# Kernel optimization log

Hardware: AMD Instinct MI355X
Metric: run time of the kernel (lower is better)

The kernel has to match this reference:

```python
import jax, jax.numpy as jnp
import numpy as np

B, L, D, H = 2, 2048, 1024, 16
DH = D // H  # 64


def setup_inputs() -> dict:
    key = jax.random.key(0)
    ks = jax.random.split(key, 9)
    s = 1.0 / np.sqrt(D)
    x = jax.random.normal(ks[0], (B, L, D), dtype=jnp.float32)
    # per-head projection weights stacked on leading head axis (torch Linear: y = x W^T + b)
    Wq = jax.random.normal(ks[1], (H, D, DH), dtype=jnp.float32) * s
    bq = jax.random.normal(ks[2], (H, DH), dtype=jnp.float32) * s
    Wk = jax.random.normal(ks[3], (H, D, DH), dtype=jnp.float32) * s
    bk = jax.random.normal(ks[4], (H, DH), dtype=jnp.float32) * s
    Wv = jax.random.normal(ks[5], (H, D, DH), dtype=jnp.float32) * s
    bv = jax.random.normal(ks[6], (H, DH), dtype=jnp.float32) * s
    WO = jax.random.normal(ks[7], (D, D), dtype=jnp.float32) * s  # torch layout [out, in]
    bO = jax.random.normal(ks[8], (D,), dtype=jnp.float32) * s
    return {"x": x, "Wq": Wq, "bq": bq, "Wk": Wk, "bk": bk,
            "Wv": Wv, "bv": bv, "WO": WO, "bO": bO}


def reference(x, Wq, bq, Wk, bk, Wv, bv, WO, bO):
    # Q,K,V: [B,H,L,DH]
    Q = jnp.einsum('bld,hdk->bhlk', x, Wq) + bq[None, :, None, :]
    K = jnp.einsum('bld,hdk->bhlk', x, Wk) + bk[None, :, None, :]
    V = jnp.einsum('bld,hdk->bhlk', x, Wv) + bv[None, :, None, :]
    scale = 1.0 / jnp.sqrt(jnp.asarray(DH, dtype=x.dtype))
    att = jnp.einsum('bhik,bhjk->bhij', Q, K) * scale  # [B,H,Lq,Lk]
    # NOTE: original softmaxes over dim=1 of [B,Lq,Lk] -> the QUERY axis (axis=2 here)
    att = jax.nn.softmax(att, axis=2)
    # dropout is identity in eval/reference mode
    out = jnp.einsum('bhij,bhjk->bhik', att, V)  # [B,H,L,DH]
    out = out.transpose(0, 2, 1, 3).reshape(B, L, D)  # concat heads on feature axis
    return jnp.einsum('bld,ed->ble', out, WO) + bO
```

## Files before the change

kernel.cpp:

```cpp
#include <hip/hip_runtime.h>
#include <math.h>

#define NB 2
#define NL 2048
#define ND 1024
#define NH 16
#define NDH 64
static constexpr float SCALE = 0.125f;

typedef short          bhalf8 __attribute__((ext_vector_type(8)));
typedef unsigned short ush8   __attribute__((ext_vector_type(8)));
typedef unsigned short ush4   __attribute__((ext_vector_type(4)));
typedef float          f32x4  __attribute__((ext_vector_type(4)));

#define MFMA_BF16(a, b, c) __builtin_amdgcn_mfma_f32_16x16x32_bf16(a, b, c, 0, 0, 0)

__device__ __forceinline__ unsigned short f2bf(float f) {
    unsigned u = __float_as_uint(f);
    u += 0x7FFF + ((u >> 16) & 1);
    return (unsigned short)(u >> 16);
}
__device__ __forceinline__ float bf2f(unsigned short s) {
    return __uint_as_float((unsigned)s << 16);
}
__device__ __forceinline__ unsigned pack_bf16(float lo, float hi) {
    unsigned a = __float_as_uint(lo) + 0x8000u;
    unsigned b = __float_as_uint(hi) + 0x8000u;
    return __builtin_amdgcn_perm(b, a, 0x07060302u);
}
__device__ __forceinline__ void gload16(const unsigned short* g, unsigned short* l) {
    __builtin_amdgcn_global_load_lds(
        (const __attribute__((address_space(1))) unsigned int*)(const void*)g,
        (__attribute__((address_space(3))) unsigned int*)(void*)l,
        16, 0, 0);
}

__global__ __launch_bounds__(256) void k_cvt(
    const float* __restrict__ x, const float* __restrict__ WO,
    unsigned short* __restrict__ xb, unsigned short* __restrict__ wob)
{
    size_t u = (size_t)blockIdx.x * 256 + threadIdx.x;
    const float* src; unsigned short* dst; size_t off;
    if (u < 524288) { src = x;  dst = xb;  off = u * 8; }
    else            { src = WO; dst = wob; off = (u - 524288) * 8; }
    float4 a = *(const float4*)(src + off);
    float4 b = *(const float4*)(src + off + 4);
    uint4 o;
    o.x = pack_bf16(a.x, a.y); o.y = pack_bf16(a.z, a.w);
    o.z = pack_bf16(b.x, b.y); o.w = pack_bf16(b.z, b.w);
    *(uint4*)(dst + off) = o;
}

__global__ __launch_bounds__(256) void k_cvt_wt(
    const float* __restrict__ Wq, const float* __restrict__ Wk,
    const float* __restrict__ Wv, unsigned short* __restrict__ Wtb)
{
    __shared__ unsigned short T[64][72];
    const int d0  = blockIdx.x * 64;
    const int qkv = blockIdx.y >> 4;
    const int h   = blockIdx.y & 15;
    const float* W = (qkv == 0 ? Wq : (qkv == 1 ? Wk : Wv)) + (size_t)h * (ND * NDH);
    const int t = threadIdx.x;
#pragma unroll
    for (int p = 0; p < 4; ++p) {
        int u  = t + p * 256;
        int dr = u >> 4;
        int c4 = (u & 15) * 4;
        float4 v = *(const float4*)(W + (size_t)(d0 + dr) * NDH + c4);
        T[c4 + 0][dr] = f2bf(v.x);
        T[c4 + 1][dr] = f2bf(v.y);
        T[c4 + 2][dr] = f2bf(v.z);
        T[c4 + 3][dr] = f2bf(v.w);
    }
    __syncthreads();
    unsigned short* outp = Wtb + (size_t)(qkv * NH + h) * NDH * ND;
#pragma unroll
    for (int p = 0; p < 2; ++p) {
        int u  = t + p * 256;
        int dh = u >> 3;
        int sg = (u & 7) * 8;
        *(ush8*)(outp + (size_t)dh * ND + d0 + sg) = *(ush8*)&T[dh][sg];
    }
}

__global__ __launch_bounds__(256, 2) void k_qkv_mfma(
    const unsigned short* __restrict__ xb, const unsigned short* __restrict__ Wtb,
    const float* __restrict__ bq, const float* __restrict__ bk,
    const float* __restrict__ bv,
    unsigned short* __restrict__ Qb, unsigned short* __restrict__ Kb,
    unsigned short* __restrict__ Vtb)
{
    __shared__ unsigned short LB[2 * 128 * 64];
    unsigned short* As = LB;
    unsigned short* Bs = LB + 128 * 64;

    const int mt = blockIdx.x;
    const int nt = blockIdx.y;
    const int qkv = nt >> 3;
    const int t = threadIdx.x, w = t >> 6, lane = t & 63;
    const int lr = lane & 15, lg = lane >> 4;
    const int wm = (w >> 1) * 64, wn = (w & 1) * 64;
    const int swz = (lr & 7) << 3;
    const int rA = lane >> 3, cg = (lane & 7) * 8;

    f32x4 acc[4][4] = {};

    for (int k0 = 0; k0 < ND; k0 += 64) {
        __syncthreads();
#pragma unroll
        for (int i = 0; i < 4; ++i) {
            int c  = w * 4 + i;
            int r  = c * 8 + rA;
            int gc = cg ^ ((r & 7) << 3);
            gload16(xb  + (size_t)(mt * 128 + r) * ND + k0 + gc, &As[c * 512]);
            gload16(Wtb + (size_t)(nt * 128 + r) * ND + k0 + gc, &Bs[c * 512]);
        }
        __syncthreads();

        bhalf8 av[4][2], bw[4][2];
#pragma unroll
        for (int f = 0; f < 4; ++f)
#pragma unroll
            for (int ks = 0; ks < 2; ++ks) {
                int c = (ks * 32 + lg * 8) ^ swz;
                av[f][ks] = *(const bhalf8*)&As[(wm + f * 16 + lr) * 64 + c];
                bw[f][ks] = *(const bhalf8*)&Bs[(wn + f * 16 + lr) * 64 + c];
            }
#pragma unroll
        for (int mf = 0; mf < 4; ++mf)
#pragma unroll
            for (int nf = 0; nf < 4; ++nf) {
                acc[mf][nf] = MFMA_BF16(av[mf][0], bw[nf][0], acc[mf][nf]);
                acc[mf][nf] = MFMA_BF16(av[mf][1], bw[nf][1], acc[mf][nf]);
            }
    }

    const float* bias = (qkv == 0 ? bq : (qkv == 1 ? bk : bv));
    const int nb = (nt & 7) * 128;
    float bi[4];
#pragma unroll
    for (int nf = 0; nf < 4; ++nf) bi[nf] = bias[nb + wn + nf * 16 + lr];

    __syncthreads();
    unsigned short* TS = LB;

    if (qkv < 2) {
#pragma unroll
        for (int mf = 0; mf < 4; ++mf)
#pragma unroll
            for (int nf = 0; nf < 4; ++nf)
#pragma unroll
                for (int r = 0; r < 4; ++r) {
                    int m = wm + mf * 16 + lg * 4 + r;
                    int n = (wn + nf * 16 + lr) ^ ((m & 7) << 3);
                    TS[m * 128 + n] = f2bf(acc[mf][nf][r] + bi[nf]);
                }
        __syncthreads();
        unsigned short* outp = (qkv == 0 ? Qb : Kb);
#pragma unroll
        for (int p = 0; p < 8; ++p) {
            int u = t + p * 256;
            int r = u >> 4, sg = (u & 15) * 8;
            ush8 v = *(const ush8*)&TS[r * 128 + (sg ^ ((r & 7) << 3))];
            int m = mt * 128 + r;
            int b = m >> 11, l = m & (NL - 1);
            int n = nb + sg;
            int h = n >> 6, dh = n & 63;
            *(ush8*)(outp + ((size_t)(b * NH + h) * NL + l) * NDH + dh) = v;
        }
    } else {
#pragma unroll
        for (int mf = 0; mf < 4; ++mf)
#pragma unroll
            for (int nf = 0; nf < 4; ++nf) {
                int n = wn + nf * 16 + lr;
                int mc = (wm + mf * 16 + lg * 4) ^ ((n & 7) << 3);
                ush4 pk;
#pragma unroll
                for (int r = 0; r < 4; ++r) pk[r] = f2bf(acc[mf][nf][r] + bi[nf]);
                *(ush4*)&TS[n * 128 + mc] = pk;
            }
        __syncthreads();
#pragma unroll
        for (int p = 0; p < 8; ++p) {
            int u = t + p * 256;
            int r = u >> 4, sg = (u & 15) * 8;
            ush8 v = *(const ush8*)&TS[r * 128 + (sg ^ ((r & 7) << 3))];
            int n = nb + r;
            int h = n >> 6, dh = n & 63;
            int m0 = mt * 128 + sg;
            int b = m0 >> 11, l0 = m0 & (NL - 1);
            *(ush8*)(Vtb + ((size_t)(b * NH + h) * NDH + dh) * NL + l0) = v;
        }
    }
}

__global__ __launch_bounds__(512) void k_colsum_mfma(
    const unsigned short* __restrict__ Qb, const unsigned short* __restrict__ Kb,
    unsigned short* __restrict__ Vtb)
{
    __shared__ unsigned short Ks[128 * 64];
    __shared__ unsigned short Qs[64 * 64];
    __shared__ float zpart[2][128];
    __shared__ float rzbuf[128];

    const int jt = blockIdx.x;
    const int bh = blockIdx.y;
    const unsigned short* Qp = Qb + (size_t)bh * NL * NDH;
    const unsigned short* Kp = Kb + (size_t)bh * NL * NDH;
    const int t = threadIdx.x, w = t >> 6, lane = t & 63;
    const int lr = lane & 15, lg = lane >> 4;
    const int jg = w & 3;
    const int ig = w >> 2;
    const int swz = (lr & 7) << 3;
    const int rA = lane >> 3, cg = (lane & 7) * 8;

#pragma unroll
    for (int i = 0; i < 2; ++i) {
        int c  = w * 2 + i;
        int r  = c * 8 + rA;
        int gc = cg ^ ((r & 7) << 3);
        gload16(Kp + (size_t)(jt * 128 + r) * NDH + gc, &Ks[c * 512]);
    }
    __syncthreads();
    bhalf8 kf[2][2];
#pragma unroll
    for (int jf = 0; jf < 2; ++jf)
#pragma unroll
        for (int ks = 0; ks < 2; ++ks)
            kf[jf][ks] = *(const bhalf8*)&Ks[(jg * 32 + jf * 16 + lr) * 64 +
                                            ((ks * 32 + lg * 8) ^ swz)];

    float zacc[2][4] = {};

    for (int it = 0; it < 32; ++it) {
        __syncthreads();
        {
            int r  = w * 8 + rA;
            int gc = cg ^ ((r & 7) << 3);
            gload16(Qp + (size_t)(it * 64 + r) * NDH + gc, &Qs[w * 512]);
        }
        __syncthreads();

#pragma unroll
        for (int ii = 0; ii < 2; ++ii) {
            bhalf8 q0 = *(const bhalf8*)&Qs[(ig * 32 + ii * 16 + lr) * 64 + ((lg * 8) ^ swz)];
            bhalf8 q1 = *(const bhalf8*)&Qs[(ig * 32 + ii * 16 + lr) * 64 + ((32 + lg * 8) ^ swz)];
#pragma unroll
            for (int jf = 0; jf < 2; ++jf) {
                f32x4 s = {};
                s = MFMA_BF16(kf[jf][0], q0, s);
                s = MFMA_BF16(kf[jf][1], q1, s);
#pragma unroll
                for (int r = 0; r < 4; ++r) zacc[jf][r] += __expf(s[r] * SCALE);
            }
        }
    }

#pragma unroll
    for (int jf = 0; jf < 2; ++jf)
#pragma unroll
        for (int r = 0; r < 4; ++r) {
            float v = zacc[jf][r];
            v += __shfl_xor(v, 1);
            v += __shfl_xor(v, 2);
            v += __shfl_xor(v, 4);
            v += __shfl_xor(v, 8);
            if (lr == 0) zpart[ig][jg * 32 + jf * 16 + lg * 4 + r] = v;
        }
    __syncthreads();
    if (t < 128) rzbuf[t] = 1.0f / (zpart[0][t] + zpart[1][t]);
    __syncthreads();

    unsigned short* Vp = Vtb + (size_t)bh * NDH * NL + jt * 128;
    {
        int dh = t >> 3, jj = (t & 7) * 16;
        unsigned short* vp = Vp + (size_t)dh * NL + jj;
        ush8 v0 = *(const ush8*)vp;
        ush8 v1 = *(const ush8*)(vp + 8);
        float4 z0 = *(const float4*)&rzbuf[jj];
        float4 z1 = *(const float4*)&rzbuf[jj + 4];
        float4 z2 = *(const float4*)&rzbuf[jj + 8];
        float4 z3 = *(const float4*)&rzbuf[jj + 12];
        uint4 o0, o1;
        o0.x = pack_bf16(bf2f(v0[0]) * z0.x, bf2f(v0[1]) * z0.y);
        o0.y = pack_bf16(bf2f(v0[2]) * z0.z, bf2f(v0[3]) * z0.w);
        o0.z = pack_bf16(bf2f(v0[4]) * z1.x, bf2f(v0[5]) * z1.y);
        o0.w = pack_bf16(bf2f(v0[6]) * z1.z, bf2f(v0[7]) * z1.w);
        o1.x = pack_bf16(bf2f(v1[0]) * z2.x, bf2f(v1[1]) * z2.y);
        o1.y = pack_bf16(bf2f(v1[2]) * z2.z, bf2f(v1[3]) * z2.w);
        o1.z = pack_bf16(bf2f(v1[4]) * z3.x, bf2f(v1[5]) * z3.y);
        o1.w = pack_bf16(bf2f(v1[6]) * z3.z, bf2f(v1[7]) * z3.w);
        *(uint4*)vp = o0;
        *(uint4*)(vp + 8) = o1;
    }
}

__global__ __launch_bounds__(512) void k_av_mfma(
    const unsigned short* __restrict__ Qb, const unsigned short* __restrict__ Kb,
    const unsigned short* __restrict__ Vtb, unsigned short* __restrict__ AOb)
{
    __shared__ unsigned short Qs[128 * 64];
    __shared__ unsigned short Ks[64 * 64];
    __shared__ unsigned short Vts[64 * 64];
    __shared__ unsigned short Ps[128 * 64];

    const int it = blockIdx.x;
    const int bh = blockIdx.y;
    const int b = bh >> 4, h = bh & 15;
    const unsigned short* Qp = Qb  + (size_t)bh * NL * NDH;
    const unsigned short* Kp = Kb  + (size_t)bh * NL * NDH;
    const unsigned short* Vp = Vtb + (size_t)bh * NDH * NL;

    const int t = threadIdx.x, w = t >> 6, lane = t & 63;
    const int lr = lane & 15, lg = lane >> 4;
    const int jgS = w & 1;
    const int igS = w >> 1;
    const int swz = (lr & 7) << 3;
    const int rA = lane >> 3, cg = (lane & 7) * 8;

#pragma unroll
    for (int i = 0; i < 2; ++i) {
        int c  = w * 2 + i;
        int r  = c * 8 + rA;
        int gc = cg ^ ((r & 7) << 3);
        gload16(Qp + (size_t)(it * 128 + r) * NDH + gc, &Qs[c * 512]);
    }
    __syncthreads();
    bhalf8 qf[2][2];
#pragma unroll
    for (int ii = 0; ii < 2; ++ii)
#pragma unroll
        for (int ks = 0; ks < 2; ++ks)
            qf[ii][ks] = *(const bhalf8*)&Qs[(igS * 32 + ii * 16 + lr) * 64 +
                                            ((ks * 32 + lg * 8) ^ swz)];

    f32x4 oacc[2][4] = {};

    for (int jt = 0; jt < 32; ++jt) {
        __syncthreads();
        {
            int r  = w * 8 + rA;
            int gc = cg ^ ((r & 7) << 3);
            gload16(Kp + (size_t)(jt * 64 + r) * NDH + gc, &Ks[w * 512]);
            gload16(Vp + (size_t)r * NL + jt * 64 + gc,    &Vts[w * 512]);
        }
        __syncthreads();

#pragma unroll
        for (int jf = 0; jf < 2; ++jf) {
            bhalf8 k0 = *(const bhalf8*)&Ks[(jgS * 32 + jf * 16 + lr) * 64 + ((lg * 8) ^ swz)];
            bhalf8 k1 = *(const bhalf8*)&Ks[(jgS * 32 + jf * 16 + lr) * 64 + ((32 + lg * 8) ^ swz)];
#pragma unroll
            for (int ii = 0; ii < 2; ++ii) {
                f32x4 s = {};
                s = MFMA_BF16(k0, qf[ii][0], s);
                s = MFMA_BF16(k1, qf[ii][1], s);
                uint2 pk;
                pk.x = pack_bf16(__expf(s[0] * SCALE), __expf(s[1] * SCALE));
                pk.y = pack_bf16(__expf(s[2] * SCALE), __expf(s[3] * SCALE));
                int i = igS * 32 + ii * 16 + lr;
                *(uint2*)&Ps[i * 64 + ((jgS * 32 + jf * 16 + lg * 4) ^ ((i & 7) << 3))] = pk;
            }
        }
        __syncthreads();

        if (w < 4) {
            bhalf8 pa[2][2];
#pragma unroll
            for (int iif = 0; iif < 2; ++iif)
#pragma unroll
                for (int ks = 0; ks < 2; ++ks)
                    pa[iif][ks] = *(const bhalf8*)&Ps[(w * 32 + iif * 16 + lr) * 64 +
                                                     ((ks * 32 + lg * 8) ^ swz)];
#pragma unroll
            for (int nf = 0; nf < 4; ++nf) {
                bhalf8 v0 = *(const bhalf8*)&Vts[(nf * 16 + lr) * 64 + ((lg * 8) ^ swz)];
                bhalf8 v1 = *(const bhalf8*)&Vts[(nf * 16 + lr) * 64 + ((32 + lg * 8) ^ swz)];
#pragma unroll
                for (int iif = 0; iif < 2; ++iif) {
                    oacc[iif][nf] = MFMA_BF16(pa[iif][0], v0, oacc[iif][nf]);
                    oacc[iif][nf] = MFMA_BF16(pa[iif][1], v1, oacc[iif][nf]);
                }
            }
        }
    }

    __syncthreads();
    if (w < 4) {
#pragma unroll
        for (int iif = 0; iif < 2; ++iif)
#pragma unroll
            for (int nf = 0; nf < 4; ++nf)
#pragma unroll
                for (int r = 0; r < 4; ++r) {
                    int li  = w * 32 + iif * 16 + lg * 4 + r;
                    int dhc = (nf * 16 + lr) ^ ((li & 7) << 3);
                    Ps[li * 64 + dhc] = f2bf(oacc[iif][nf][r]);
                }
    }
    __syncthreads();
    {
        int r = t >> 2, sgq = (t & 3) * 16;
        int sz2 = (r & 7) << 3;
        ush8 v0 = *(const ush8*)&Ps[r * 64 + (sgq ^ sz2)];
        ush8 v1 = *(const ush8*)&Ps[r * 64 + ((sgq + 8) ^ sz2)];
        unsigned short* op = AOb + ((size_t)(b * NL + it * 128 + r)) * ND + h * NDH + sgq;
        *(ush8*)op = v0;
        *(ush8*)(op + 8) = v1;
    }
}

__global__ __launch_bounds__(256, 2) void k_oproj_mfma(
    const unsigned short* __restrict__ AOb, const unsigned short* __restrict__ WOb,
    const float* __restrict__ bO, float* __restrict__ y)
{
    __shared__ unsigned short As[64 * 64];
    __shared__ unsigned short Bs[128 * 64];

    const int mt = blockIdx.x;
    const int nt = blockIdx.y;
    const int t = threadIdx.x, w = t >> 6, lane = t & 63;
    const int lr = lane & 15, lg = lane >> 4;
    const int wn = w * 32;
    const int swz = (lr & 7) << 3;
    const int rA = lane >> 3, cg = (lane & 7) * 8;

    f32x4 acc[4][2] = {};

    for (int k0 = 0; k0 < ND; k0 += 64) {
        __syncthreads();
#pragma unroll
        for (int i = 0; i < 2; ++i) {
            int c  = w * 2 + i;
            int r  = c * 8 + rA;
            int gc = cg ^ ((r & 7) << 3);
            gload16(AOb + (size_t)(mt * 64 + r) * ND + k0 + gc, &As[c * 512]);
        }
#pragma unroll
        for (int i = 0; i < 4; ++i) {
            int c  = w * 4 + i;
            int r  = c * 8 + rA;
            int gc = cg ^ ((r & 7) << 3);
            gload16(WOb + (size_t)(nt * 128 + r) * ND + k0 + gc, &Bs[c * 512]);
        }
        __syncthreads();

        bhalf8 bw[2][2];
#pragma unroll
        for (int nf = 0; nf < 2; ++nf)
#pragma unroll
            for (int ks = 0; ks < 2; ++ks)
                bw[nf][ks] = *(const bhalf8*)&Bs[(wn + nf * 16 + lr) * 64 +
                                                ((ks * 32 + lg * 8) ^ swz)];
#pragma unroll
        for (int mf = 0; mf < 4; ++mf) {
            bhalf8 a0 = *(const bhalf8*)&As[(mf * 16 + lr) * 64 + ((lg * 8) ^ swz)];
            bhalf8 a1 = *(const bhalf8*)&As[(mf * 16 + lr) * 64 + ((32 + lg * 8) ^ swz)];
#pragma unroll
            for (int nf = 0; nf < 2; ++nf) {
                acc[mf][nf] = MFMA_BF16(a0, bw[nf][0], acc[mf][nf]);
                acc[mf][nf] = MFMA_BF16(a1, bw[nf][1], acc[mf][nf]);
            }
        }
    }

#pragma unroll
    for (int mf = 0; mf < 4; ++mf)
#pragma unroll
        for (int nf = 0; nf < 2; ++nf) {
            int e = nt * 128 + wn + nf * 16 + lr;
            float bo = bO[e];
#pragma unroll
            for (int r = 0; r < 4; ++r) {
                int m = mt * 64 + mf * 16 + lg * 4 + r;
                y[(size_t)m * ND + e] = acc[mf][nf][r] + bo;
            }
        }
}

extern "C" void kernel_launch(void* const* d_in, const int* in_sizes, int n_in,
                              void* d_out, int out_size, void* d_ws, size_t ws_size,
                              hipStream_t stream)
{
    const float* x  = (const float*)d_in[0];
    const float* Wq = (const float*)d_in[1];
    const float* bq = (const float*)d_in[2];
    const float* Wk = (const float*)d_in[3];
    const float* bk = (const float*)d_in[4];
    const float* Wv = (const float*)d_in[5];
    const float* bv = (const float*)d_in[6];
    const float* WO = (const float*)d_in[7];
    const float* bO = (const float*)d_in[8];
    float* y = (float*)d_out;

    unsigned short* xb  = (unsigned short*)d_ws;
    unsigned short* Wtb = xb  + 4194304;
    unsigned short* WOb = Wtb + 3145728;
    unsigned short* Qb  = WOb + 1048576;
    unsigned short* Kb  = Qb  + 4194304;
    unsigned short* Vtb = Kb  + 4194304;
    unsigned short* AOb = Vtb + 4194304;

    hipLaunchKernelGGL(k_cvt,         dim3(2560),   dim3(256), 0, stream, x, WO, xb, WOb);
    hipLaunchKernelGGL(k_cvt_wt,      dim3(16, 48), dim3(256), 0, stream, Wq, Wk, Wv, Wtb);
    hipLaunchKernelGGL(k_qkv_mfma,    dim3(32, 24), dim3(256), 0, stream,
                       xb, Wtb, bq, bk, bv, Qb, Kb, Vtb);
    hipLaunchKernelGGL(k_colsum_mfma, dim3(16, 32), dim3(512), 0, stream, Qb, Kb, Vtb);
    hipLaunchKernelGGL(k_av_mfma,     dim3(16, 32), dim3(512), 0, stream, Qb, Kb, Vtb, AOb);
    hipLaunchKernelGGL(k_oproj_mfma,  dim3(64, 8),  dim3(256), 0, stream, AOb, WOb, bO, y);
}
```

Measured before the change: 215.1 us.

## Double-buffer LDS tiles in all GEMM/attention kernels and fold softmax scale into Wq

Result: no change. 218.0 us (+1.4%).

```diff
diff --git a/kernel.cpp b/kernel.cpp
--- a/kernel.cpp
+++ b/kernel.cpp
@@ -6,7 +6,7 @@
 #define ND 1024
 #define NH 16
 #define NDH 64
-static constexpr float SCALE = 0.125f;
+static constexpr float QSCL = 0.18033688011112042f;
 
 typedef short          bhalf8 __attribute__((ext_vector_type(8)));
 typedef unsigned short ush8   __attribute__((ext_vector_type(8)));
@@ -33,6 +33,18 @@
         (const __attribute__((address_space(1))) unsigned int*)(const void*)g,
         (__attribute__((address_space(3))) unsigned int*)(void*)l,
         16, 0, 0);
+}
+__device__ __forceinline__ void sync_vm0() {
+    asm volatile("s_waitcnt vmcnt(0)" ::: "memory");
+    __builtin_amdgcn_sched_barrier(0);
+    __builtin_amdgcn_s_barrier();
+    __builtin_amdgcn_sched_barrier(0);
+}
+__device__ __forceinline__ void sync_lgkm0() {
+    asm volatile("s_waitcnt lgkmcnt(0)" ::: "memory");
+    __builtin_amdgcn_sched_barrier(0);
+    __builtin_amdgcn_s_barrier();
+    __builtin_amdgcn_sched_barrier(0);
 }
 
 __global__ __launch_bounds__(256) void k_cvt(
@@ -60,6 +72,7 @@
     const int qkv = blockIdx.y >> 4;
     const int h   = blockIdx.y & 15;
     const float* W = (qkv == 0 ? Wq : (qkv == 1 ? Wk : Wv)) + (size_t)h * (ND * NDH);
+    const float sc = (qkv == 0) ? QSCL : 1.0f;
     const int t = threadIdx.x;
 #pragma unroll
     for (int p = 0; p < 4; ++p) {
@@ -67,10 +80,10 @@
         int dr = u >> 4;
         int c4 = (u & 15) * 4;
         float4 v = *(const float4*)(W + (size_t)(d0 + dr) * NDH + c4);
-        T[c4 + 0][dr] = f2bf(v.x);
-        T[c4 + 1][dr] = f2bf(v.y);
-        T[c4 + 2][dr] = f2bf(v.z);
-        T[c4 + 3][dr] = f2bf(v.w);
+        T[c4 + 0][dr] = f2bf(v.x * sc);
+        T[c4 + 1][dr] = f2bf(v.y * sc);
+        T[c4 + 2][dr] = f2bf(v.z * sc);
+        T[c4 + 3][dr] = f2bf(v.w * sc);
     }
     __syncthreads();
     unsigned short* outp = Wtb + (size_t)(qkv * NH + h) * NDH * ND;
@@ -90,9 +103,8 @@
     unsigned short* __restrict__ Qb, unsigned short* __restrict__ Kb,
     unsigned short* __restrict__ Vtb)
 {
-    __shared__ unsigned short LB[2 * 128 * 64];
-    unsigned short* As = LB;
-    unsigned short* Bs = LB + 128 * 64;
+    constexpr int CH = 128 * 64;
+    __shared__ unsigned short LB[4 * CH];
 
     const int mt = blockIdx.x;
     const int nt = blockIdx.y;
@@ -103,19 +115,26 @@
     const int swz = (lr & 7) << 3;
     const int rA = lane >> 3, cg = (lane & 7) * 8;
 
-    f32x4 acc[4][4] = {};
-
-    for (int k0 = 0; k0 < ND; k0 += 64) {
-        __syncthreads();
+    auto stage = [&](int k0, int buf) {
 #pragma unroll
         for (int i = 0; i < 4; ++i) {
             int c  = w * 4 + i;
             int r  = c * 8 + rA;
             int gc = cg ^ ((r & 7) << 3);
-            gload16(xb  + (size_t)(mt * 128 + r) * ND + k0 + gc, &As[c * 512]);
-            gload16(Wtb + (size_t)(nt * 128 + r) * ND + k0 + gc, &Bs[c * 512]);
-        }
-        __syncthreads();
+            gload16(xb  + (size_t)(mt * 128 + r) * ND + k0 + gc, LB + buf * CH + c * 512);
+            gload16(Wtb + (size_t)(nt * 128 + r) * ND + k0 + gc, LB + (2 + buf) * CH + c * 512);
+        }
+    };
+
+    f32x4 acc[4][4] = {};
+    stage(0, 0);
+    sync_vm0();
+
+    int cur = 0;
+    for (int k0 = 0; k0 < ND; k0 += 64) {
+        if (k0 + 64 < ND) stage(k0 + 64, cur ^ 1);
+        const unsigned short* Ac = LB + cur * CH;
+        const unsigned short* Bc = LB + (2 + cur) * CH;
 
         bhalf8 av[4][2], bw[4][2];
 #pragma unroll
@@ -123,8 +142,8 @@
 #pragma unroll
             for (int ks = 0; ks < 2; ++ks) {
                 int c = (ks * 32 + lg * 8) ^ swz;
-                av[f][ks] = *(const bhalf8*)&As[(wm + f * 16 + lr) * 64 + c];
-                bw[f][ks] = *(const bhalf8*)&Bs[(wn + f * 16 + lr) * 64 + c];
+                av[f][ks] = *(const bhalf8*)&Ac[(wm + f * 16 + lr) * 64 + c];
+                bw[f][ks] = *(const bhalf8*)&Bc[(wn + f * 16 + lr) * 64 + c];
             }
 #pragma unroll
         for (int mf = 0; mf < 4; ++mf)
@@ -133,15 +152,17 @@
                 acc[mf][nf] = MFMA_BF16(av[mf][0], bw[nf][0], acc[mf][nf]);
                 acc[mf][nf] = MFMA_BF16(av[mf][1], bw[nf][1], acc[mf][nf]);
             }
+        sync_vm0();
+        cur ^= 1;
     }
 
     const float* bias = (qkv == 0 ? bq : (qkv == 1 ? bk : bv));
+    const float bsc = (qkv == 0) ? QSCL : 1.0f;
     const int nb = (nt & 7) * 128;
     float bi[4];
 #pragma unroll
-    for (int nf = 0; nf < 4; ++nf) bi[nf] = bias[nb + wn + nf * 16 + lr];
-
-    __syncthreads();
+    for (int nf = 0; nf < 4; ++nf) bi[nf] = bias[nb + wn + nf * 16 + lr] * bsc;
+
     unsigned short* TS = LB;
 
     if (qkv < 2) {
@@ -199,8 +220,9 @@
     const unsigned short* __restrict__ Qb, const unsigned short* __restrict__ Kb,
     unsigned short* __restrict__ Vtb)
 {
+    constexpr int CQ = 64 * 64;
     __shared__ unsigned short Ks[128 * 64];
-    __shared__ unsigned short Qs[64 * 64];
+    __shared__ unsigned short Qs[2 * CQ];
     __shared__ float zpart[2][128];
     __shared__ float rzbuf[128];
 
@@ -222,7 +244,13 @@
         int gc = cg ^ ((r & 7) << 3);
         gload16(Kp + (size_t)(jt * 128 + r) * NDH + gc, &Ks[c * 512]);
     }
-    __syncthreads();
+    {
+        int r  = w * 8 + rA;
+        int gc = cg ^ ((r & 7) << 3);
+        gload16(Qp + (size_t)r * NDH + gc, Qs + w * 512);
+    }
+    sync_vm0();
+
     bhalf8 kf[2][2];
 #pragma unroll
     for (int jf = 0; jf < 2; ++jf)
@@ -232,29 +260,29 @@
                                             ((ks * 32 + lg * 8) ^ swz)];
 
     float zacc[2][4] = {};
-
+    int cur = 0;
     for (int it = 0; it < 32; ++it) {
-        __syncthreads();
-        {
+        if (it + 1 < 32) {
             int r  = w * 8 + rA;
             int gc = cg ^ ((r & 7) << 3);
-            gload16(Qp + (size_t)(it * 64 + r) * NDH + gc, &Qs[w * 512]);
-        }
-        __syncthreads();
-
+            gload16(Qp + (size_t)((it + 1) * 64 + r) * NDH + gc, Qs + (cur ^ 1) * CQ + w * 512);
+        }
+        const unsigned short* Qc = Qs + cur * CQ;
 #pragma unroll
         for (int ii = 0; ii < 2; ++ii) {
-            bhalf8 q0 = *(const bhalf8*)&Qs[(ig * 32 + ii * 16 + lr) * 64 + ((lg * 8) ^ swz)];
-            bhalf8 q1 = *(const bhalf8*)&Qs[(ig * 32 + ii * 16 + lr) * 64 + ((32 + lg * 8) ^ swz)];
+            bhalf8 q0 = *(const bhalf8*)&Qc[(ig * 32 + ii * 16 + lr) * 64 + ((lg * 8) ^ swz)];
+            bhalf8 q1 = *(const bhalf8*)&Qc[(ig * 32 + ii * 16 + lr) * 64 + ((32 + lg * 8) ^ swz)];
 #pragma unroll
             for (int jf = 0; jf < 2; ++jf) {
                 f32x4 s = {};
                 s = MFMA_BF16(kf[jf][0], q0, s);
                 s = MFMA_BF16(kf[jf][1], q1, s);
 #pragma unroll
-                for (int r = 0; r < 4; ++r) zacc[jf][r] += __expf(s[r] * SCALE);
-            }
-        }
+                for (int r = 0; r < 4; ++r) zacc[jf][r] += __builtin_amdgcn_exp2f(s[r]);
+            }
+        }
+        sync_vm0();
+        cur ^= 1;
     }
 
 #pragma unroll
@@ -300,9 +328,10 @@
     const unsigned short* __restrict__ Qb, const unsigned short* __restrict__ Kb,
     const unsigned short* __restrict__ Vtb, unsigned short* __restrict__ AOb)
 {
+    constexpr int CK = 64 * 64;
     __shared__ unsigned short Qs[128 * 64];
-    __shared__ unsigned short Ks[64 * 64];
-    __shared__ unsigned short Vts[64 * 64];
+    __shared__ unsigned short Ks[2 * CK];
+    __shared__ unsigned short Vts[2 * CK];
     __shared__ unsigned short Ps[128 * 64];
 
     const int it = blockIdx.x;
@@ -319,6 +348,13 @@
     const int swz = (lr & 7) << 3;
     const int rA = lane >> 3, cg = (lane & 7) * 8;
 
+    auto stageKV = [&](int jt, int buf) {
+        int r  = w * 8 + rA;
+        int gc = cg ^ ((r & 7) << 3);
+        gload16(Kp + (size_t)(jt * 64 + r) * NDH + gc, Ks  + buf * CK + w * 512);
+        gload16(Vp + (size_t)r * NL + jt * 64 + gc,    Vts + buf * CK + w * 512);
+    };
+
 #pragma unroll
     for (int i = 0; i < 2; ++i) {
         int c  = w * 2 + i;
@@ -326,7 +362,9 @@
         int gc = cg ^ ((r & 7) << 3);
         gload16(Qp + (size_t)(it * 128 + r) * NDH + gc, &Qs[c * 512]);
     }
-    __syncthreads();
+    stageKV(0, 0);
+    sync_vm0();
+
     bhalf8 qf[2][2];
 #pragma unroll
     for (int ii = 0; ii < 2; ++ii)
@@ -336,36 +374,32 @@
                                             ((ks * 32 + lg * 8) ^ swz)];
 
     f32x4 oacc[2][4] = {};
+    int cur = 0;
 
     for (int jt = 0; jt < 32; ++jt) {
-        __syncthreads();
-        {
-            int r  = w * 8 + rA;
-            int gc = cg ^ ((r & 7) << 3);
-            gload16(Kp + (size_t)(jt * 64 + r) * NDH + gc, &Ks[w * 512]);
-            gload16(Vp + (size_t)r * NL + jt * 64 + gc,    &Vts[w * 512]);
-        }
-        __syncthreads();
-
+        if (jt + 1 < 32) stageKV(jt + 1, cur ^ 1);
+
+        const unsigned short* Kc = Ks + cur * CK;
 #pragma unroll
         for (int jf = 0; jf < 2; ++jf) {
-            bhalf8 k0 = *(const bhalf8*)&Ks[(jgS * 32 + jf * 16 + lr) * 64 + ((lg * 8) ^ swz)];
-            bhalf8 k1 = *(const bhalf8*)&Ks[(jgS * 32 + jf * 16 + lr) * 64 + ((32 + lg * 8) ^ swz)];
+            bhalf8 k0 = *(const bhalf8*)&Kc[(jgS * 32 + jf * 16 + lr) * 64 + ((lg * 8) ^ swz)];
+            bhalf8 k1 = *(const bhalf8*)&Kc[(jgS * 32 + jf * 16 + lr) * 64 + ((32 + lg * 8) ^ swz)];
 #pragma unroll
             for (int ii = 0; ii < 2; ++ii) {
                 f32x4 s = {};
                 s = MFMA_BF16(k0, qf[ii][0], s);
                 s = MFMA_BF16(k1, qf[ii][1], s);
                 uint2 pk;
-                pk.x = pack_bf16(__expf(s[0] * SCALE), __expf(s[1] * SCALE));
-                pk.y = pack_bf16(__expf(s[2] * SCALE), __expf(s[3] * SCALE));
+                pk.x = pack_bf16(__builtin_amdgcn_exp2f(s[0]), __builtin_amdgcn_exp2f(s[1]));
+                pk.y = pack_bf16(__builtin_amdgcn_exp2f(s[2]), __builtin_amdgcn_exp2f(s[3]));
                 int i = igS * 32 + ii * 16 + lr;
                 *(uint2*)&Ps[i * 64 + ((jgS * 32 + jf * 16 + lg * 4) ^ ((i & 7) << 3))] = pk;
             }
         }
-        __syncthreads();
+        sync_lgkm0();
 
         if (w < 4) {
+            const unsigned short* Vc = Vts + cur * CK;
             bhalf8 pa[2][2];
 #pragma unroll
             for (int iif = 0; iif < 2; ++iif)
@@ -373,20 +407,26 @@
                 for (int ks = 0; ks < 2; ++ks)
                     pa[iif][ks] = *(const bhalf8*)&Ps[(w * 32 + iif * 16 + lr) * 64 +
                                                      ((ks * 32 + lg * 8) ^ swz)];
+            bhalf8 vb0[4], vb1[4];
 #pragma unroll
             for (int nf = 0; nf < 4; ++nf) {
-                bhalf8 v0 = *(const bhalf8*)&Vts[(nf * 16 + lr) * 64 + ((lg * 8) ^ swz)];
-                bhalf8 v1 = *(const bhalf8*)&Vts[(nf * 16 + lr) * 64 + ((32 + lg * 8) ^ swz)];
+                vb0[nf] = *(const bhalf8*)&Vc[(nf * 16 + lr) * 64 + ((lg * 8) ^ swz)];
+                vb1[nf] = *(const bhalf8*)&Vc[(nf * 16 + lr) * 64 + ((32 + lg * 8) ^ swz)];
+            }
+            __builtin_amdgcn_s_setprio(1);
+#pragma unroll
+            for (int nf = 0; nf < 4; ++nf)
 #pragma unroll
                 for (int iif = 0; iif < 2; ++iif) {
-                    oacc[iif][nf] = MFMA_BF16(pa[iif][0], v0, oacc[iif][nf]);
-                    oacc[iif][nf] = MFMA_BF16(pa[iif][1], v1, oacc[iif][nf]);
+                    oacc[iif][nf] = MFMA_BF16(pa[iif][0], vb0[nf], oacc[iif][nf]);
+                    oacc[iif][nf] = MFMA_BF16(pa[iif][1], vb1[nf], oacc[iif][nf]);
                 }
-            }
-        }
-    }
-
-    __syncthreads();
+            __builtin_amdgcn_s_setprio(0);
+        }
+        sync_vm0();
+        cur ^= 1;
+    }
+
     if (w < 4) {
 #pragma unroll
         for (int iif = 0; iif < 2; ++iif)
@@ -415,8 +455,9 @@
     const unsigned short* __restrict__ AOb, const unsigned short* __restrict__ WOb,
     const float* __restrict__ bO, float* __restrict__ y)
 {
-    __shared__ unsigned short As[64 * 64];
-    __shared__ unsigned short Bs[128 * 64];
+    constexpr int CA = 64 * 64, CB = 128 * 64;
+    __shared__ unsigned short As[2 * CA];
+    __shared__ unsigned short Bs[2 * CB];
 
     const int mt = blockIdx.x;
     const int nt = blockIdx.y;
@@ -426,43 +467,52 @@
     const int swz = (lr & 7) << 3;
     const int rA = lane >> 3, cg = (lane & 7) * 8;
 
-    f32x4 acc[4][2] = {};
-
-    for (int k0 = 0; k0 < ND; k0 += 64) {
-        __syncthreads();
+    auto stage = [&](int k0, int buf) {
 #pragma unroll
         for (int i = 0; i < 2; ++i) {
             int c  = w * 2 + i;
             int r  = c * 8 + rA;
             int gc = cg ^ ((r & 7) << 3);
-            gload16(AOb + (size_t)(mt * 64 + r) * ND + k0 + gc, &As[c * 512]);
+            gload16(AOb + (size_t)(mt * 64 + r) * ND + k0 + gc, As + buf * CA + c * 512);
         }
 #pragma unroll
         for (int i = 0; i < 4; ++i) {
             int c  = w * 4 + i;
             int r  = c * 8 + rA;
             int gc = cg ^ ((r & 7) << 3);
-            gload16(WOb + (size_t)(nt * 128 + r) * ND + k0 + gc, &Bs[c * 512]);
-        }
-        __syncthreads();
+            gload16(WOb + (size_t)(nt * 128 + r) * ND + k0 + gc, Bs + buf * CB + c * 512);
+        }
+    };
+
+    f32x4 acc[4][2] = {};
+    stage(0, 0);
+    sync_vm0();
+
+    int cur = 0;
+    for (int k0 = 0; k0 < ND; k0 += 64) {
+        if (k0 + 64 < ND) stage(k0 + 64, cur ^ 1);
+        const unsigned short* Ac = As + cur * CA;
+        const unsigned short* Bc = Bs + cur * CB;
 
         bhalf8 bw[2][2];
 #pragma unroll
         for (int nf = 0; nf < 2; ++nf)
 #pragma unroll
             for (int ks = 0; ks < 2; ++ks)
-                bw[nf][ks] = *(const bhalf8*)&Bs[(wn + nf * 16 + lr) * 64 +
+                bw[nf][ks] = *(const bhalf8*)&Bc[(wn + nf * 16 + lr) * 64 +
                                                 ((ks * 32 + lg * 8) ^ swz)];
 #pragma unroll
         for (int mf = 0; mf < 4; ++mf) {
-            bhalf8 a0 = *(const bhalf8*)&As[(mf * 16 + lr) * 64 + ((lg * 8) ^ swz)];
-            bhalf8 a1 = *(const bhalf8*)&As[(mf * 16 + lr) * 64 + ((32 + lg * 8) ^ swz)];
+            bhalf8 a0 = *(const bhalf8*)&Ac[(mf * 16 + lr) * 64 + ((lg * 8) ^ swz)];
+            bhalf8 a1 = *(const bhalf8*)&Ac[(mf * 16 + lr) * 64 + ((32 + lg * 8) ^ swz)];
 #pragma unroll
             for (int nf = 0; nf < 2; ++nf) {
                 acc[mf][nf] = MFMA_BF16(a0, bw[nf][0], acc[mf][nf]);
                 acc[mf][nf] = MFMA_BF16(a1, bw[nf][1], acc[mf][nf]);
             }
         }
+        sync_vm0();
+        cur ^= 1;
     }
 
 #pragma unroll
```
